# Kernel tuning notes

Hardware: AMD Instinct MI355X
Metric: run time of the kernel (lower is better)

The kernel has to match this reference:

```python
import jax, jax.numpy as jnp
import numpy as np

NUM_NODES = 100000
NUM_EDGES = 1600000
IN_DIM = 128
HID = 128
OUT_DIM = 5


def setup_inputs() -> dict:
    key = jax.random.key(0)
    ks = jax.random.split(key, 8)
    x = jax.random.normal(ks[0], (NUM_NODES, IN_DIM), dtype=jnp.float32)
    edges = jax.random.randint(ks[1], (2, NUM_EDGES), 0, NUM_NODES, dtype=jnp.int32)
    s = 1.0 / np.sqrt(IN_DIM)
    W1 = jax.random.uniform(ks[2], (IN_DIM, HID), jnp.float32, -s, s)
    b1 = jax.random.uniform(ks[3], (HID,), jnp.float32, -s, s)
    sh = 1.0 / np.sqrt(HID)
    W2 = jax.random.uniform(ks[4], (HID, HID), jnp.float32, -sh, sh)
    b2 = jax.random.uniform(ks[5], (HID,), jnp.float32, -sh, sh)
    Wp = jax.random.uniform(ks[6], (HID, OUT_DIM), jnp.float32, -sh, sh)
    bp = jax.random.uniform(ks[7], (OUT_DIM,), jnp.float32, -sh, sh)
    return {"x": x, "edges": edges, "W1": W1, "b1": b1, "W2": W2, "b2": b2, "Wp": Wp, "bp": bp}


def _gnn_layer(x, src, tgt, W, b):
    # scatter-add of source features into targets (mean aggregation)
    agg = jax.ops.segment_sum(x[src], tgt, num_segments=NUM_NODES)  # [N, d]
    cnt = jax.ops.segment_sum(jnp.ones_like(tgt, dtype=x.dtype), tgt, num_segments=NUM_NODES)
    cnt = jnp.maximum(cnt, 1.0)  # clamp(min=1)
    agg = agg / cnt[:, None]
    combined = x + agg  # residual
    return jax.nn.relu(combined @ W + b)


def reference(x, edges, W1, b1, W2, b2, Wp, bp):
    src, tgt = edges[0], edges[1]
    h = _gnn_layer(x, src, tgt, W1, b1)
    h = _gnn_layer(h, src, tgt, W2, b2)
    return h @ Wp + bp  # [N, OUT_DIM]
```

## Files before the change

### kernel.cpp

```cpp
#include <hip/hip_runtime.h>

typedef unsigned int uint32;
typedef unsigned short ushort16;

typedef __attribute__((ext_vector_type(8))) short short8;
typedef __attribute__((ext_vector_type(4))) float f32x4;

#define BMAX 512


__device__ __forceinline__ ushort16 f2bf(float f) {
    uint32 u = __float_as_uint(f);
    u += 0x7fffu + ((u >> 16) & 1u);
    return (ushort16)(u >> 16);
}
__device__ __forceinline__ float bfhi(uint32 u) { return __uint_as_float(u & 0xffff0000u); }
__device__ __forceinline__ float bflo(uint32 u) { return __uint_as_float(u << 16); }
__device__ __forceinline__ uint32 pack2(float a, float b) {
    return (uint32)f2bf(a) | ((uint32)f2bf(b) << 16);
}

union U16 { uint4 u; short8 s; };
__device__ __forceinline__ short8 ld_frag(const ushort16* p) {
    U16 x; x.u = *(const uint4*)p; return x.s;
}

__global__ void prep_wt_kernel(const float* __restrict__ W1, const float* __restrict__ W2,
                               ushort16* __restrict__ Wt1, ushort16* __restrict__ Wt2) {
    const float* W = blockIdx.x ? W2 : W1;
    ushort16* Wt = blockIdx.x ? Wt2 : Wt1;
    for (int i = threadIdx.x; i < 16384; i += 256) {
        int k = i >> 7, c = i & 127;
        Wt[c * 128 + k] = f2bf(W[i]);
    }
}

__global__ __launch_bounds__(256)
void hist_cvt_kernel(const int* __restrict__ tgt, int* __restrict__ hist,
                     const float* __restrict__ x, uint4* __restrict__ xb,
                     int E, int C, int B, int G1, int n64) {
    __shared__ int lh[BMAX];
    int tid = threadIdx.x, blk = blockIdx.x;
    for (int b = tid; b < B; b += 256) lh[b] = 0;
    __syncthreads();
    int e0 = blk * C, e1 = min(e0 + C, E);
    for (int e = e0 + tid; e < e1; e += 256)
        atomicAdd(&lh[tgt[e] >> 8], 1);
    for (int i = blk * 256 + tid; i < n64; i += G1 * 256) {
        const float4* p = (const float4*)x + (size_t)i * 16;
        uint4* q = xb + (size_t)i * 8;
#pragma unroll
        for (int j = 0; j < 8; ++j) {
            float4 a = p[2 * j], bb = p[2 * j + 1];
            uint4 o;
            o.x = pack2(a.x, a.y); o.y = pack2(a.z, a.w);
            o.z = pack2(bb.x, bb.y); o.w = pack2(bb.z, bb.w);
            q[j] = o;
        }
    }
    __syncthreads();
    for (int b = tid; b < B; b += 256) hist[blk * B + b] = lh[b];
}

__global__ __launch_bounds__(256)
void colscan_kernel(int* __restrict__ hist, int* __restrict__ total, int G1, int B) {
    __shared__ int sd[256];
    __shared__ int carrySh;
    int b = blockIdx.x, tid = threadIdx.x;
    if (tid == 0) carrySh = 0;
    __syncthreads();
    for (int g0 = 0; g0 < G1; g0 += 256) {
        int g = g0 + tid;
        int v = (g < G1) ? hist[g * B + b] : 0;
        int c0 = carrySh;
        sd[tid] = v;
        __syncthreads();
        for (int o = 1; o < 256; o <<= 1) {
            int t = (tid >= o) ? sd[tid - o] : 0;
            __syncthreads();
            sd[tid] += t;
            __syncthreads();
        }
        if (g < G1) hist[g * B + b] = sd[tid] - v + c0;
        int tot = sd[255];
        __syncthreads();
        if (tid == 0) carrySh = c0 + tot;
        __syncthreads();
    }
    if (tid == 0) total[b] = carrySh;
}

__global__ __launch_bounds__(512)
void bucketstart_kernel(const int* __restrict__ total, int* __restrict__ bucketStart, int B) {
    __shared__ int sd[512];
    int tid = threadIdx.x;
    int v = (tid < B) ? total[tid] : 0;
    sd[tid] = v;
    __syncthreads();
    for (int o = 1; o < 512; o <<= 1) {
        int t = (tid >= o) ? sd[tid - o] : 0;
        __syncthreads();
        sd[tid] += t;
        __syncthreads();
    }
    if (tid < B) bucketStart[tid] = sd[tid] - v;
    if (tid == 511) bucketStart[B] = sd[511];
}

__global__ __launch_bounds__(256)
void partition_kernel(const int* __restrict__ src, const int* __restrict__ tgt,
                      const int* __restrict__ hist, const int* __restrict__ bucketStart,
                      int2* __restrict__ ebuf, int E, int C, int B) {
    __shared__ int cur[BMAX];
    int tid = threadIdx.x, blk = blockIdx.x;
    for (int b = tid; b < B; b += 256) cur[b] = hist[blk * B + b] + bucketStart[b];
    __syncthreads();
    int e0 = blk * C, e1 = min(e0 + C, E);
    for (int e = e0 + tid; e < e1; e += 256) {
        int t = tgt[e], s = src[e];
        int slot = atomicAdd(&cur[t >> 8], 1);
        int2 p; p.x = t; p.y = s;
        ebuf[slot] = p;
    }
}

__global__ __launch_bounds__(256)
void csr_kernel(const int2* __restrict__ ebuf, const int* __restrict__ bucketStart,
                int* __restrict__ offsets, int* __restrict__ csr, int N, int B, int E) {
    __shared__ int cnt[256];
    __shared__ int sd[256];
    int b = blockIdx.x, tid = threadIdx.x;
    int s = bucketStart[b], e1 = bucketStart[b + 1];
    int n = e1 - s, t0 = b << 8;
    cnt[tid] = 0;
    __syncthreads();
    for (int i = tid; i < n; i += 256) atomicAdd(&cnt[ebuf[s + i].x - t0], 1);
    __syncthreads();
    int v = cnt[tid];
    sd[tid] = v;
    __syncthreads();
    for (int o = 1; o < 256; o <<= 1) {
        int t = (tid >= o) ? sd[tid - o] : 0;
        __syncthreads();
        sd[tid] += t;
        __syncthreads();
    }
    int excl = sd[tid] - v;
    int t = t0 + tid;
    if (t < N) offsets[t] = s + excl;
    if (b == B - 1 && tid == 255) offsets[N] = E;
    __syncthreads();
    cnt[tid] = s + excl;
    __syncthreads();
    for (int i = tid; i < n; i += 256) {
        int2 e = ebuf[s + i];
        int slot = atomicAdd(&cnt[e.x - t0], 1);
        csr[slot] = e.y;
    }
}

__global__ __launch_bounds__(256, 4)
void agg_combine_bf16_kernel(const ushort16* __restrict__ hb,
                             const int* __restrict__ offsets, const int* __restrict__ csr,
                             uint32* __restrict__ outb, int N) {
    int wid = (blockIdx.x * 256 + threadIdx.x) >> 6;
    int lane = threadIdx.x & 63;
    if (wid >= N) return;
    int g = lane >> 4, sl = lane & 15;
    int s0 = offsets[wid];
    int deg = offsets[wid + 1] - s0;
    int fi = sl * 4 + g;
    uint32 su = ((const uint32*)hb)[(size_t)wid * 64 + fi];

    float acc[8];
#pragma unroll
    for (int j = 0; j < 8; ++j) acc[j] = 0.f;

    int base = 0;
    for (; base + 8 <= deg; base += 8) {
        int i0 = csr[s0 + base + g];
        int i1 = csr[s0 + base + 4 + g];
        uint4 v0 = *(const uint4*)(hb + (size_t)i0 * 128 + sl * 8);
        uint4 v1 = *(const uint4*)(hb + (size_t)i1 * 128 + sl * 8);
        acc[0] += bflo(v0.x); acc[1] += bfhi(v0.x);
        acc[2] += bflo(v0.y); acc[3] += bfhi(v0.y);
        acc[4] += bflo(v0.z); acc[5] += bfhi(v0.z);
        acc[6] += bflo(v0.w); acc[7] += bfhi(v0.w);
        acc[0] += bflo(v1.x); acc[1] += bfhi(v1.x);
        acc[2] += bflo(v1.y); acc[3] += bfhi(v1.y);
        acc[4] += bflo(v1.z); acc[5] += bfhi(v1.z);
        acc[6] += bflo(v1.w); acc[7] += bfhi(v1.w);
    }
    for (; base < deg; base += 4) {
        int e = base + g;
        if (e < deg) {
            int s = csr[s0 + e];
            uint4 v = *(const uint4*)(hb + (size_t)s * 128 + sl * 8);
            acc[0] += bflo(v.x); acc[1] += bfhi(v.x);
            acc[2] += bflo(v.y); acc[3] += bfhi(v.y);
            acc[4] += bflo(v.z); acc[5] += bfhi(v.z);
            acc[6] += bflo(v.w); acc[7] += bfhi(v.w);
        }
    }
#pragma unroll
    for (int j = 0; j < 8; ++j) {
        acc[j] += __shfl_xor(acc[j], 16, 64);
        acc[j] += __shfl_xor(acc[j], 32, 64);
    }
    float inv = 1.f / fmaxf((float)deg, 1.f);
    float ax = (g == 0) ? acc[0] : (g == 1) ? acc[2] : (g == 2) ? acc[4] : acc[6];
    float ay = (g == 0) ? acc[1] : (g == 1) ? acc[3] : (g == 2) ? acc[5] : acc[7];
    outb[(size_t)wid * 64 + fi] = pack2(bflo(su) + ax * inv, bfhi(su) + ay * inv);
}

__global__ __launch_bounds__(256)
void gemm_mfma_kernel(const ushort16* __restrict__ A, const ushort16* __restrict__ Wt,
                      const float* __restrict__ bias, int M,
                      ushort16* __restrict__ outB,
                      const float* __restrict__ Wp, const float* __restrict__ bp,
                      float* __restrict__ outP) {
    const int tid = threadIdx.x;
    const int lane = tid & 63;
    const int wave = tid >> 6;
    const int l15 = lane & 15;
    const int quad = lane >> 4;
    const int r0 = blockIdx.x * 64 + wave * 16;

    int arow = r0 + l15;
    if (arow >= M) arow = M - 1;
    const ushort16* aptr = A + (size_t)arow * 128 + quad * 8;
    short8 afr[4];
#pragma unroll
    for (int kt = 0; kt < 4; ++kt) afr[kt] = ld_frag(aptr + kt * 32);

    f32x4 acc[8];
#pragma unroll
    for (int t = 0; t < 8; ++t) acc[t] = (f32x4){0.f, 0.f, 0.f, 0.f};

#pragma unroll
    for (int t = 0; t < 8; ++t) {
        const ushort16* bptr = Wt + (size_t)(16 * t + l15) * 128 + quad * 8;
        short8 b0 = ld_frag(bptr);
        short8 b1 = ld_frag(bptr + 32);
        short8 b2 = ld_frag(bptr + 64);
        short8 b3 = ld_frag(bptr + 96);
        acc[t] = __builtin_amdgcn_mfma_f32_16x16x32_bf16(afr[0], b0, acc[t], 0, 0, 0);
        acc[t] = __builtin_amdgcn_mfma_f32_16x16x32_bf16(afr[1], b1, acc[t], 0, 0, 0);
        acc[t] = __builtin_amdgcn_mfma_f32_16x16x32_bf16(afr[2], b2, acc[t], 0, 0, 0);
        acc[t] = __builtin_amdgcn_mfma_f32_16x16x32_bf16(afr[3], b3, acc[t], 0, 0, 0);
    }

    if (outP) {
        float wpl[8][5];
#pragma unroll
        for (int t = 0; t < 8; ++t)
#pragma unroll
            for (int j = 0; j < 5; ++j) wpl[t][j] = Wp[(16 * t + l15) * 5 + j];
        float p[4][5];
#pragma unroll
        for (int r = 0; r < 4; ++r)
#pragma unroll
            for (int j = 0; j < 5; ++j) p[r][j] = 0.f;
#pragma unroll
        for (int t = 0; t < 8; ++t) {
            float bt = bias[16 * t + l15];
            float ov[4];
            ov[0] = fmaxf(acc[t].x + bt, 0.f);
            ov[1] = fmaxf(acc[t].y + bt, 0.f);
            ov[2] = fmaxf(acc[t].z + bt, 0.f);
            ov[3] = fmaxf(acc[t].w + bt, 0.f);
#pragma unroll
            for (int r = 0; r < 4; ++r)
#pragma unroll
                for (int j = 0; j < 5; ++j) p[r][j] += ov[r] * wpl[t][j];
        }
#pragma unroll
        for (int m = 1; m <= 8; m <<= 1)
#pragma unroll
            for (int r = 0; r < 4; ++r)
#pragma unroll
                for (int j = 0; j < 5; ++j) p[r][j] += __shfl_xor(p[r][j], m, 64);
        if (l15 == 0) {
#pragma unroll
            for (int r = 0; r < 4; ++r) {
                int row = r0 + quad * 4 + r;
                if (row < M) {
#pragma unroll
                    for (int j = 0; j < 5; ++j) outP[(size_t)row * 5 + j] = p[r][j] + bp[j];
                }
            }
        }
    } else {
#pragma unroll
        for (int t = 0; t < 8; ++t) {
            float bt = bias[16 * t + l15];
            float ov[4];
            ov[0] = fmaxf(acc[t].x + bt, 0.f);
            ov[1] = fmaxf(acc[t].y + bt, 0.f);
            ov[2] = fmaxf(acc[t].z + bt, 0.f);
            ov[3] = fmaxf(acc[t].w + bt, 0.f);
#pragma unroll
            for (int r = 0; r < 4; ++r) {
                float nb = __shfl_xor(ov[r], 1, 64);
                int row = r0 + quad * 4 + r;
                if (((l15 & 1) == 0) && row < M) {
                    *(uint32*)(outB + (size_t)row * 128 + 16 * t + l15) = pack2(ov[r], nb);
                }
            }
        }
    }
}

extern "C" void kernel_launch(void* const* d_in, const int* in_sizes, int n_in,
                              void* d_out, int out_size, void* d_ws, size_t ws_size,
                              hipStream_t stream) {
    const float* x     = (const float*)d_in[0];
    const int*   edges = (const int*)d_in[1];
    const float* W1    = (const float*)d_in[2];
    const float* b1    = (const float*)d_in[3];
    const float* W2    = (const float*)d_in[4];
    const float* b2    = (const float*)d_in[5];
    const float* Wp    = (const float*)d_in[6];
    const float* bp    = (const float*)d_in[7];
    float* out = (float*)d_out;

    const int N = in_sizes[0] / 128;
    const int E = in_sizes[1] / 2;
    const int* src = edges;
    const int* tgt = edges + E;

    const int B  = (N + 255) >> 8;
    const int C  = 2048;
    const int G1 = (E + C - 1) / C;
    const int n64 = N * 2;

    char* ws = (char*)d_ws;
    size_t off = 0;
    auto alloc = [&](size_t bytes) {
        char* p = ws + off;
        off = (off + bytes + 255) & ~(size_t)255;
        return p;
    };
    int*      offsets     = (int*)alloc((size_t)(N + 1) * 4);
    int*      csr         = (int*)alloc((size_t)E * 4);
    ushort16* xb          = (ushort16*)alloc((size_t)N * 128 * 2);
    ushort16* hb1         = (ushort16*)alloc((size_t)N * 128 * 2);
    ushort16* bufAb       = (ushort16*)alloc((size_t)N * 128 * 2);
    ushort16* Wt1         = (ushort16*)alloc(128 * 128 * 2);
    ushort16* Wt2         = (ushort16*)alloc(128 * 128 * 2);
    int*      hist        = (int*)alloc((size_t)G1 * B * 4);
    int*      total       = (int*)alloc((size_t)B * 4);
    int*      bucketStart = (int*)alloc((size_t)(B + 1) * 4);
    int2*     ebuf        = (int2*)bufAb;
    (void)ws_size;

    prep_wt_kernel<<<2, 256, 0, stream>>>(W1, W2, Wt1, Wt2);
    hist_cvt_kernel<<<G1, 256, 0, stream>>>(tgt, hist, x, (uint4*)xb, E, C, B, G1, n64);
    colscan_kernel<<<B, 256, 0, stream>>>(hist, total, G1, B);
    bucketstart_kernel<<<1, 512, 0, stream>>>(total, bucketStart, B);
    partition_kernel<<<G1, 256, 0, stream>>>(src, tgt, hist, bucketStart, ebuf, E, C, B);
    csr_kernel<<<B, 256, 0, stream>>>(ebuf, bucketStart, offsets, csr, N, B, E);

    const int aggBlocks  = (N + 3) / 4;
    const int gemmBlocks = (N + 63) / 64;

    agg_combine_bf16_kernel<<<aggBlocks, 256, 0, stream>>>(xb, offsets, csr, (uint32*)bufAb, N);
    gemm_mfma_kernel<<<gemmBlocks, 256, 0, stream>>>(bufAb, Wt1, b1, N, hb1,
                                                     nullptr, nullptr, nullptr);
    agg_combine_bf16_kernel<<<aggBlocks, 256, 0, stream>>>(hb1, offsets, csr, (uint32*)bufAb, N);
    gemm_mfma_kernel<<<gemmBlocks, 256, 0, stream>>>(bufAb, Wt2, b2, N, nullptr,
                                                     Wp, bp, out);
}
```

Measured before the change: 394.2 us.

## Fuse neighbor aggregation into MFMA GEMM via swizzled LDS tile; pack edge buffer

Merges the mean-aggregation kernel and the GEMM kernel into one per-layer kernel. Each block aggregates 64 nodes into an XOR-swizzled shared-memory tile and feeds that tile straight to the MFMA fragments, which removes the round trip of the combined activations through global memory and two launches. The edge partition buffer is packed into 32 bits (local target in the top byte, source in the low 24 bits), halving partition and CSR traffic, and the gather loop is unrolled to 16 edges. In exchange, each wave processes 16 nodes serially, so there are fewer waves in flight to hide gather latency. The 24-bit source packing assumes fewer than 16M nodes.

```diff
diff --git a/kernel.cpp b/kernel.cpp
--- a/kernel.cpp
+++ b/kernel.cpp
@@ -24,6 +24,12 @@
 __device__ __forceinline__ short8 ld_frag(const ushort16* p) {
     U16 x; x.u = *(const uint4*)p; return x.s;
 }
+
+#define ACC8(v) \
+    acc[0] += bflo(v.x); acc[1] += bfhi(v.x); \
+    acc[2] += bflo(v.y); acc[3] += bfhi(v.y); \
+    acc[4] += bflo(v.z); acc[5] += bfhi(v.z); \
+    acc[6] += bflo(v.w); acc[7] += bfhi(v.w);
 
 __global__ void prep_wt_kernel(const float* __restrict__ W1, const float* __restrict__ W2,
                                ushort16* __restrict__ Wt1, ushort16* __restrict__ Wt2) {
@@ -110,7 +116,7 @@
 __global__ __launch_bounds__(256)
 void partition_kernel(const int* __restrict__ src, const int* __restrict__ tgt,
                       const int* __restrict__ hist, const int* __restrict__ bucketStart,
-                      int2* __restrict__ ebuf, int E, int C, int B) {
+                      uint32* __restrict__ ebuf, int E, int C, int B) {
     __shared__ int cur[BMAX];
     int tid = threadIdx.x, blk = blockIdx.x;
     for (int b = tid; b < B; b += 256) cur[b] = hist[blk * B + b] + bucketStart[b];
@@ -119,13 +125,12 @@
     for (int e = e0 + tid; e < e1; e += 256) {
         int t = tgt[e], s = src[e];
         int slot = atomicAdd(&cur[t >> 8], 1);
-        int2 p; p.x = t; p.y = s;
-        ebuf[slot] = p;
+        ebuf[slot] = ((uint32)(t & 255) << 24) | (uint32)s;
     }
 }
 
 __global__ __launch_bounds__(256)
-void csr_kernel(const int2* __restrict__ ebuf, const int* __restrict__ bucketStart,
+void csr_kernel(const uint32* __restrict__ ebuf, const int* __restrict__ bucketStart,
                 int* __restrict__ offsets, int* __restrict__ csr, int N, int B, int E) {
     __shared__ int cnt[256];
     __shared__ int sd[256];
@@ -134,7 +139,7 @@
     int n = e1 - s, t0 = b << 8;
     cnt[tid] = 0;
     __syncthreads();
-    for (int i = tid; i < n; i += 256) atomicAdd(&cnt[ebuf[s + i].x - t0], 1);
+    for (int i = tid; i < n; i += 256) atomicAdd(&cnt[ebuf[s + i] >> 24], 1);
     __syncthreads();
     int v = cnt[tid];
     sd[tid] = v;
@@ -153,85 +158,87 @@
     cnt[tid] = s + excl;
     __syncthreads();
     for (int i = tid; i < n; i += 256) {
-        int2 e = ebuf[s + i];
-        int slot = atomicAdd(&cnt[e.x - t0], 1);
-        csr[slot] = e.y;
+        uint32 e = ebuf[s + i];
+        int slot = atomicAdd(&cnt[e >> 24], 1);
+        csr[slot] = (int)(e & 0x00FFFFFFu);
     }
 }
 
 __global__ __launch_bounds__(256, 4)
-void agg_combine_bf16_kernel(const ushort16* __restrict__ hb,
-                             const int* __restrict__ offsets, const int* __restrict__ csr,
-                             uint32* __restrict__ outb, int N) {
-    int wid = (blockIdx.x * 256 + threadIdx.x) >> 6;
-    int lane = threadIdx.x & 63;
-    if (wid >= N) return;
-    int g = lane >> 4, sl = lane & 15;
-    int s0 = offsets[wid];
-    int deg = offsets[wid + 1] - s0;
-    int fi = sl * 4 + g;
-    uint32 su = ((const uint32*)hb)[(size_t)wid * 64 + fi];
-
-    float acc[8];
-#pragma unroll
-    for (int j = 0; j < 8; ++j) acc[j] = 0.f;
-
-    int base = 0;
-    for (; base + 8 <= deg; base += 8) {
-        int i0 = csr[s0 + base + g];
-        int i1 = csr[s0 + base + 4 + g];
-        uint4 v0 = *(const uint4*)(hb + (size_t)i0 * 128 + sl * 8);
-        uint4 v1 = *(const uint4*)(hb + (size_t)i1 * 128 + sl * 8);
-        acc[0] += bflo(v0.x); acc[1] += bfhi(v0.x);
-        acc[2] += bflo(v0.y); acc[3] += bfhi(v0.y);
-        acc[4] += bflo(v0.z); acc[5] += bfhi(v0.z);
-        acc[6] += bflo(v0.w); acc[7] += bfhi(v0.w);
-        acc[0] += bflo(v1.x); acc[1] += bfhi(v1.x);
-        acc[2] += bflo(v1.y); acc[3] += bfhi(v1.y);
-        acc[4] += bflo(v1.z); acc[5] += bfhi(v1.z);
-        acc[6] += bflo(v1.w); acc[7] += bfhi(v1.w);
-    }
-    for (; base < deg; base += 4) {
-        int e = base + g;
-        if (e < deg) {
-            int s = csr[s0 + e];
-            uint4 v = *(const uint4*)(hb + (size_t)s * 128 + sl * 8);
-            acc[0] += bflo(v.x); acc[1] += bfhi(v.x);
-            acc[2] += bflo(v.y); acc[3] += bfhi(v.y);
-            acc[4] += bflo(v.z); acc[5] += bfhi(v.z);
-            acc[6] += bflo(v.w); acc[7] += bfhi(v.w);
-        }
-    }
-#pragma unroll
-    for (int j = 0; j < 8; ++j) {
-        acc[j] += __shfl_xor(acc[j], 16, 64);
-        acc[j] += __shfl_xor(acc[j], 32, 64);
-    }
-    float inv = 1.f / fmaxf((float)deg, 1.f);
-    float ax = (g == 0) ? acc[0] : (g == 1) ? acc[2] : (g == 2) ? acc[4] : acc[6];
-    float ay = (g == 0) ? acc[1] : (g == 1) ? acc[3] : (g == 2) ? acc[5] : acc[7];
-    outb[(size_t)wid * 64 + fi] = pack2(bflo(su) + ax * inv, bfhi(su) + ay * inv);
-}
-
-__global__ __launch_bounds__(256)
-void gemm_mfma_kernel(const ushort16* __restrict__ A, const ushort16* __restrict__ Wt,
-                      const float* __restrict__ bias, int M,
-                      ushort16* __restrict__ outB,
-                      const float* __restrict__ Wp, const float* __restrict__ bp,
-                      float* __restrict__ outP) {
+void fused_layer_kernel(const ushort16* __restrict__ hb,
+                        const int* __restrict__ offsets, const int* __restrict__ csr,
+                        const ushort16* __restrict__ Wt, const float* __restrict__ bias,
+                        int N,
+                        ushort16* __restrict__ outB,
+                        const float* __restrict__ Wp, const float* __restrict__ bp,
+                        float* __restrict__ outP) {
+    __shared__ uint32 comb[64 * 64];
     const int tid = threadIdx.x;
     const int lane = tid & 63;
     const int wave = tid >> 6;
-    const int l15 = lane & 15;
-    const int quad = lane >> 4;
-    const int r0 = blockIdx.x * 64 + wave * 16;
-
-    int arow = r0 + l15;
-    if (arow >= M) arow = M - 1;
-    const ushort16* aptr = A + (size_t)arow * 128 + quad * 8;
+    const int g = lane >> 4, sl = lane & 15;
+    const int n0 = blockIdx.x * 64;
+
+    for (int i = 0; i < 16; ++i) {
+        int lr = wave * 16 + i;
+        int node = n0 + lr;
+        int chunk = sl ^ (lr & 7);
+        uint32* dst = &comb[lr * 64 + chunk * 4 + g];
+        if (node < N) {
+            int s0 = offsets[node];
+            int deg = offsets[node + 1] - s0;
+            uint32 su = ((const uint32*)hb)[(size_t)node * 64 + sl * 4 + g];
+            float acc[8];
+#pragma unroll
+            for (int j = 0; j < 8; ++j) acc[j] = 0.f;
+            int base = 0;
+            for (; base + 16 <= deg; base += 16) {
+                int i0 = csr[s0 + base + g];
+                int i1 = csr[s0 + base + 4 + g];
+                int i2 = csr[s0 + base + 8 + g];
+                int i3 = csr[s0 + base + 12 + g];
+                uint4 v0 = *(const uint4*)(hb + (size_t)i0 * 128 + sl * 8);
+                uint4 v1 = *(const uint4*)(hb + (size_t)i1 * 128 + sl * 8);
+                uint4 v2 = *(const uint4*)(hb + (size_t)i2 * 128 + sl * 8);
+                uint4 v3 = *(const uint4*)(hb + (size_t)i3 * 128 + sl * 8);
+                ACC8(v0); ACC8(v1); ACC8(v2); ACC8(v3);
+            }
+            for (; base < deg; base += 4) {
+                int e = base + g;
+                if (e < deg) {
+                    int s = csr[s0 + e];
+                    uint4 v = *(const uint4*)(hb + (size_t)s * 128 + sl * 8);
+                    ACC8(v);
+                }
+            }
+#pragma unroll
+            for (int j = 0; j < 8; ++j) {
+                acc[j] += __shfl_xor(acc[j], 16, 64);
+                acc[j] += __shfl_xor(acc[j], 32, 64);
+            }
+            float inv = 1.f / fmaxf((float)deg, 1.f);
+            float ax = (g == 0) ? acc[0] : (g == 1) ? acc[2] : (g == 2) ? acc[4] : acc[6];
+            float ay = (g == 0) ? acc[1] : (g == 1) ? acc[3] : (g == 2) ? acc[5] : acc[7];
+            *dst = pack2(bflo(su) + ax * inv, bfhi(su) + ay * inv);
+        } else {
+            *dst = 0;
+        }
+    }
+    __syncthreads();
+
+    const int l15 = sl;
+    const int quad = g;
+    const int lr0 = wave * 16;
+    const int myrow = lr0 + l15;
+
     short8 afr[4];
 #pragma unroll
-    for (int kt = 0; kt < 4; ++kt) afr[kt] = ld_frag(aptr + kt * 32);
+    for (int kt = 0; kt < 4; ++kt) {
+        int chunk = (quad + kt * 4) ^ (myrow & 7);
+        U16 x;
+        x.u = *(const uint4*)&comb[myrow * 64 + chunk * 4];
+        afr[kt] = x.s;
+    }
 
     f32x4 acc[8];
 #pragma unroll
@@ -251,16 +258,44 @@
     }
 
     if (outP) {
-        float wpl[8][5];
-#pragma unroll
-        for (int t = 0; t < 8; ++t)
-#pragma unroll
-            for (int j = 0; j < 5; ++j) wpl[t][j] = Wp[(16 * t + l15) * 5 + j];
         float p[4][5];
 #pragma unroll
         for (int r = 0; r < 4; ++r)
 #pragma unroll
             for (int j = 0; j < 5; ++j) p[r][j] = 0.f;
+#pragma unroll
+        for (int t = 0; t < 8; ++t) {
+            float wpl[5];
+#pragma unroll
+            for (int j = 0; j < 5; ++j) wpl[j] = Wp[(16 * t + l15) * 5 + j];
+            float bt = bias[16 * t + l15];
+            float ov[4];
+            ov[0] = fmaxf(acc[t].x + bt, 0.f);
+            ov[1] = fmaxf(acc[t].y + bt, 0.f);
+            ov[2] = fmaxf(acc[t].z + bt, 0.f);
+            ov[3] = fmaxf(acc[t].w + bt, 0.f);
+#pragma unroll
+            for (int r = 0; r < 4; ++r)
+#pragma unroll
+                for (int j = 0; j < 5; ++j) p[r][j] += ov[r] * wpl[j];
+        }
+#pragma unroll
+        for (int m = 1; m <= 8; m <<= 1)
+#pragma unroll
+            for (int r = 0; r < 4; ++r)
+#pragma unroll
+                for (int j = 0; j < 5; ++j) p[r][j] += __shfl_xor(p[r][j], m, 64);
+        if (l15 == 0) {
+#pragma unroll
+            for (int r = 0; r < 4; ++r) {
+                int row = n0 + lr0 + quad * 4 + r;
+                if (row < N) {
+#pragma unroll
+                    for (int j = 0; j < 5; ++j) outP[(size_t)row * 5 + j] = p[r][j] + bp[j];
+                }
+            }
+        }
+    } else {
 #pragma unroll
         for (int t = 0; t < 8; ++t) {
             float bt = bias[16 * t + l15];
@@ -270,40 +305,10 @@
             ov[2] = fmaxf(acc[t].z + bt, 0.f);
             ov[3] = fmaxf(acc[t].w + bt, 0.f);
 #pragma unroll
-            for (int r = 0; r < 4; ++r)
-#pragma unroll
-                for (int j = 0; j < 5; ++j) p[r][j] += ov[r] * wpl[t][j];
-        }
-#pragma unroll
-        for (int m = 1; m <= 8; m <<= 1)
-#pragma unroll
-            for (int r = 0; r < 4; ++r)
-#pragma unroll
-                for (int j = 0; j < 5; ++j) p[r][j] += __shfl_xor(p[r][j], m, 64);
-        if (l15 == 0) {
-#pragma unroll
-            for (int r = 0; r < 4; ++r) {
-                int row = r0 + quad * 4 + r;
-                if (row < M) {
-#pragma unroll
-                    for (int j = 0; j < 5; ++j) outP[(size_t)row * 5 + j] = p[r][j] + bp[j];
-                }
-            }
-        }
-    } else {
-#pragma unroll
-        for (int t = 0; t < 8; ++t) {
-            float bt = bias[16 * t + l15];
-            float ov[4];
-            ov[0] = fmaxf(acc[t].x + bt, 0.f);
-            ov[1] = fmaxf(acc[t].y + bt, 0.f);
-            ov[2] = fmaxf(acc[t].z + bt, 0.f);
-            ov[3] = fmaxf(acc[t].w + bt, 0.f);
-#pragma unroll
             for (int r = 0; r < 4; ++r) {
                 float nb = __shfl_xor(ov[r], 1, 64);
-                int row = r0 + quad * 4 + r;
-                if (((l15 & 1) == 0) && row < M) {
+                int row = n0 + lr0 + quad * 4 + r;
+                if (((l15 & 1) == 0) && row < N) {
                     *(uint32*)(outB + (size_t)row * 128 + 16 * t + l15) = pack2(ov[r], nb);
                 }
             }
@@ -345,13 +350,12 @@
     int*      csr         = (int*)alloc((size_t)E * 4);
     ushort16* xb          = (ushort16*)alloc((size_t)N * 128 * 2);
     ushort16* hb1         = (ushort16*)alloc((size_t)N * 128 * 2);
-    ushort16* bufAb       = (ushort16*)alloc((size_t)N * 128 * 2);
     ushort16* Wt1         = (ushort16*)alloc(128 * 128 * 2);
     ushort16* Wt2         = (ushort16*)alloc(128 * 128 * 2);
     int*      hist        = (int*)alloc((size_t)G1 * B * 4);
     int*      total       = (int*)alloc((size_t)B * 4);
     int*      bucketStart = (int*)alloc((size_t)(B + 1) * 4);
-    int2*     ebuf        = (int2*)bufAb;
+    uint32*   ebuf        = (uint32*)alloc((size_t)E * 4);
     (void)ws_size;
 
     prep_wt_kernel<<<2, 256, 0, stream>>>(W1, W2, Wt1, Wt2);
@@ -361,13 +365,10 @@
     partition_kernel<<<G1, 256, 0, stream>>>(src, tgt, hist, bucketStart, ebuf, E, C, B);
     csr_kernel<<<B, 256, 0, stream>>>(ebuf, bucketStart, offsets, csr, N, B, E);
 
-    const int aggBlocks  = (N + 3) / 4;
-    const int gemmBlocks = (N + 63) / 64;
-
-    agg_combine_bf16_kernel<<<aggBlocks, 256, 0, stream>>>(xb, offsets, csr, (uint32*)bufAb, N);
-    gemm_mfma_kernel<<<gemmBlocks, 256, 0, stream>>>(bufAb, Wt1, b1, N, hb1,
-                                                     nullptr, nullptr, nullptr);
-    agg_combine_bf16_kernel<<<aggBlocks, 256, 0, stream>>>(hb1, offsets, csr, (uint32*)bufAb, N);
-    gemm_mfma_kernel<<<gemmBlocks, 256, 0, stream>>>(bufAb, Wt2, b2, N, nullptr,
-                                                     Wp, bp, out);
-}
+    const int fusedBlocks = (N + 63) / 64;
+
+    fused_layer_kernel<<<fusedBlocks, 256, 0, stream>>>(
+        xb, offsets, csr, Wt1, b1, N, hb1, nullptr, nullptr, nullptr);
+    fused_layer_kernel<<<fusedBlocks, 256, 0, stream>>>(
+        hb1, offsets, csr, Wt2, b2, N, nullptr, Wp, bp, out);
+}
```

Measured after the change: 442.6 us. 12.3% more time.

## Fold weight prep and bucket scan into neighbouring kernels; pack edge buffer to 32-bit

Applied to the files above, without the earlier changes.

Merges the weight transpose/convert kernel into the histogram kernel as two extra blocks and removes the separate bucket-start scan kernel. The partition and CSR kernels now each redo the small bucket prefix scan locally. This drops two launches and their serialization gaps. The intermediate edge buffer packs the local target offset (8 bits) with the source index (24 bits) into one uint32, halving its write and read traffic, but this assumes node indices fit in 24 bits. The Wp loads in the GEMM epilogue are also moved inside the loop to cut register pressure.

```diff
diff --git a/kernel.cpp b/kernel.cpp
--- a/kernel.cpp
+++ b/kernel.cpp
@@ -25,22 +25,49 @@
     U16 x; x.u = *(const uint4*)p; return x.s;
 }
 
-__global__ void prep_wt_kernel(const float* __restrict__ W1, const float* __restrict__ W2,
-                               ushort16* __restrict__ Wt1, ushort16* __restrict__ Wt2) {
-    const float* W = blockIdx.x ? W2 : W1;
-    ushort16* Wt = blockIdx.x ? Wt2 : Wt1;
-    for (int i = threadIdx.x; i < 16384; i += 256) {
-        int k = i >> 7, c = i & 127;
-        Wt[c * 128 + k] = f2bf(W[i]);
-    }
-}
-
-__global__ __launch_bounds__(256)
-void hist_cvt_kernel(const int* __restrict__ tgt, int* __restrict__ hist,
-                     const float* __restrict__ x, uint4* __restrict__ xb,
-                     int E, int C, int B, int G1, int n64) {
+#define ACC8(v) \
+    acc[0] += bflo(v.x); acc[1] += bfhi(v.x); \
+    acc[2] += bflo(v.y); acc[3] += bfhi(v.y); \
+    acc[4] += bflo(v.z); acc[5] += bfhi(v.z); \
+    acc[6] += bflo(v.w); acc[7] += bfhi(v.w);
+
+__device__ __forceinline__ void bucket_scan(const int* __restrict__ total, int B,
+                                            int* bs , int* sd ) {
+    int tid = threadIdx.x;
+    int v0 = (2 * tid     < B) ? total[2 * tid]     : 0;
+    int v1 = (2 * tid + 1 < B) ? total[2 * tid + 1] : 0;
+    int s = v0 + v1;
+    sd[tid] = s;
+    __syncthreads();
+    for (int o = 1; o < 256; o <<= 1) {
+        int t = (tid >= o) ? sd[tid - o] : 0;
+        __syncthreads();
+        sd[tid] += t;
+        __syncthreads();
+    }
+    int excl = sd[tid] - s;
+    bs[2 * tid]     = excl;
+    bs[2 * tid + 1] = excl + v0;
+    __syncthreads();
+}
+
+__global__ __launch_bounds__(256)
+void hist_cvt_prep_kernel(const int* __restrict__ tgt, int* __restrict__ hist,
+                          const float* __restrict__ x, uint4* __restrict__ xb,
+                          const float* __restrict__ W1, const float* __restrict__ W2,
+                          ushort16* __restrict__ Wt1, ushort16* __restrict__ Wt2,
+                          int E, int C, int B, int G1, int n64) {
+    int tid = threadIdx.x, blk = blockIdx.x;
+    if (blk >= G1) {
+        const float* W = (blk - G1) ? W2 : W1;
+        ushort16* Wt = (blk - G1) ? Wt2 : Wt1;
+        for (int i = tid; i < 16384; i += 256) {
+            int k = i >> 7, c = i & 127;
+            Wt[c * 128 + k] = f2bf(W[i]);
+        }
+        return;
+    }
     __shared__ int lh[BMAX];
-    int tid = threadIdx.x, blk = blockIdx.x;
     for (int b = tid; b < B; b += 256) lh[b] = 0;
     __syncthreads();
     int e0 = blk * C, e1 = min(e0 + C, E);
@@ -90,51 +117,39 @@
     if (tid == 0) total[b] = carrySh;
 }
 
-__global__ __launch_bounds__(512)
-void bucketstart_kernel(const int* __restrict__ total, int* __restrict__ bucketStart, int B) {
-    __shared__ int sd[512];
-    int tid = threadIdx.x;
-    int v = (tid < B) ? total[tid] : 0;
-    sd[tid] = v;
-    __syncthreads();
-    for (int o = 1; o < 512; o <<= 1) {
-        int t = (tid >= o) ? sd[tid - o] : 0;
-        __syncthreads();
-        sd[tid] += t;
-        __syncthreads();
-    }
-    if (tid < B) bucketStart[tid] = sd[tid] - v;
-    if (tid == 511) bucketStart[B] = sd[511];
-}
-
 __global__ __launch_bounds__(256)
 void partition_kernel(const int* __restrict__ src, const int* __restrict__ tgt,
-                      const int* __restrict__ hist, const int* __restrict__ bucketStart,
-                      int2* __restrict__ ebuf, int E, int C, int B) {
+                      const int* __restrict__ hist, const int* __restrict__ total,
+                      uint32* __restrict__ ebuf, int E, int C, int B) {
+    __shared__ int bs[512];
+    __shared__ int sd[256];
     __shared__ int cur[BMAX];
     int tid = threadIdx.x, blk = blockIdx.x;
-    for (int b = tid; b < B; b += 256) cur[b] = hist[blk * B + b] + bucketStart[b];
+    bucket_scan(total, B, bs, sd);
+    for (int b = tid; b < B; b += 256) cur[b] = hist[blk * B + b] + bs[b];
     __syncthreads();
     int e0 = blk * C, e1 = min(e0 + C, E);
     for (int e = e0 + tid; e < e1; e += 256) {
         int t = tgt[e], s = src[e];
         int slot = atomicAdd(&cur[t >> 8], 1);
-        int2 p; p.x = t; p.y = s;
-        ebuf[slot] = p;
-    }
-}
-
-__global__ __launch_bounds__(256)
-void csr_kernel(const int2* __restrict__ ebuf, const int* __restrict__ bucketStart,
+        ebuf[slot] = ((uint32)(t & 255) << 24) | (uint32)s;
+    }
+}
+
+__global__ __launch_bounds__(256)
+void csr_kernel(const uint32* __restrict__ ebuf, const int* __restrict__ total,
                 int* __restrict__ offsets, int* __restrict__ csr, int N, int B, int E) {
+    __shared__ int bs[512];
+    __shared__ int sd[256];
     __shared__ int cnt[256];
-    __shared__ int sd[256];
     int b = blockIdx.x, tid = threadIdx.x;
-    int s = bucketStart[b], e1 = bucketStart[b + 1];
-    int n = e1 - s, t0 = b << 8;
+    bucket_scan(total, B, bs, sd);
+    int s = bs[b];
+    int n = bs[b + 1] - s;
+    int t0 = b << 8;
     cnt[tid] = 0;
     __syncthreads();
-    for (int i = tid; i < n; i += 256) atomicAdd(&cnt[ebuf[s + i].x - t0], 1);
+    for (int i = tid; i < n; i += 256) atomicAdd(&cnt[ebuf[s + i] >> 24], 1);
     __syncthreads();
     int v = cnt[tid];
     sd[tid] = v;
@@ -153,9 +168,9 @@
     cnt[tid] = s + excl;
     __syncthreads();
     for (int i = tid; i < n; i += 256) {
-        int2 e = ebuf[s + i];
-        int slot = atomicAdd(&cnt[e.x - t0], 1);
-        csr[slot] = e.y;
+        uint32 e = ebuf[s + i];
+        int slot = atomicAdd(&cnt[e >> 24], 1);
+        csr[slot] = (int)(e & 0x00FFFFFFu);
     }
 }
 
@@ -182,24 +197,14 @@
         int i1 = csr[s0 + base + 4 + g];
         uint4 v0 = *(const uint4*)(hb + (size_t)i0 * 128 + sl * 8);
         uint4 v1 = *(const uint4*)(hb + (size_t)i1 * 128 + sl * 8);
-        acc[0] += bflo(v0.x); acc[1] += bfhi(v0.x);
-        acc[2] += bflo(v0.y); acc[3] += bfhi(v0.y);
-        acc[4] += bflo(v0.z); acc[5] += bfhi(v0.z);
-        acc[6] += bflo(v0.w); acc[7] += bfhi(v0.w);
-        acc[0] += bflo(v1.x); acc[1] += bfhi(v1.x);
-        acc[2] += bflo(v1.y); acc[3] += bfhi(v1.y);
-        acc[4] += bflo(v1.z); acc[5] += bfhi(v1.z);
-        acc[6] += bflo(v1.w); acc[7] += bfhi(v1.w);
+        ACC8(v0); ACC8(v1);
     }
     for (; base < deg; base += 4) {
         int e = base + g;
         if (e < deg) {
             int s = csr[s0 + e];
             uint4 v = *(const uint4*)(hb + (size_t)s * 128 + sl * 8);
-            acc[0] += bflo(v.x); acc[1] += bfhi(v.x);
-            acc[2] += bflo(v.y); acc[3] += bfhi(v.y);
-            acc[4] += bflo(v.z); acc[5] += bfhi(v.z);
-            acc[6] += bflo(v.w); acc[7] += bfhi(v.w);
+            ACC8(v);
         }
     }
 #pragma unroll
@@ -251,11 +256,6 @@
     }
 
     if (outP) {
-        float wpl[8][5];
-#pragma unroll
-        for (int t = 0; t < 8; ++t)
-#pragma unroll
-            for (int j = 0; j < 5; ++j) wpl[t][j] = Wp[(16 * t + l15) * 5 + j];
         float p[4][5];
 #pragma unroll
         for (int r = 0; r < 4; ++r)
@@ -263,6 +263,9 @@
             for (int j = 0; j < 5; ++j) p[r][j] = 0.f;
 #pragma unroll
         for (int t = 0; t < 8; ++t) {
+            float wpl[5];
+#pragma unroll
+            for (int j = 0; j < 5; ++j) wpl[j] = Wp[(16 * t + l15) * 5 + j];
             float bt = bias[16 * t + l15];
             float ov[4];
             ov[0] = fmaxf(acc[t].x + bt, 0.f);
@@ -272,7 +275,7 @@
 #pragma unroll
             for (int r = 0; r < 4; ++r)
 #pragma unroll
-                for (int j = 0; j < 5; ++j) p[r][j] += ov[r] * wpl[t][j];
+                for (int j = 0; j < 5; ++j) p[r][j] += ov[r] * wpl[j];
         }
 #pragma unroll
         for (int m = 1; m <= 8; m <<= 1)
@@ -341,25 +344,23 @@
         off = (off + bytes + 255) & ~(size_t)255;
         return p;
     };
-    int*      offsets     = (int*)alloc((size_t)(N + 1) * 4);
-    int*      csr         = (int*)alloc((size_t)E * 4);
-    ushort16* xb          = (ushort16*)alloc((size_t)N * 128 * 2);
-    ushort16* hb1         = (ushort16*)alloc((size_t)N * 128 * 2);
-    ushort16* bufAb       = (ushort16*)alloc((size_t)N * 128 * 2);
-    ushort16* Wt1         = (ushort16*)alloc(128 * 128 * 2);
-    ushort16* Wt2         = (ushort16*)alloc(128 * 128 * 2);
-    int*      hist        = (int*)alloc((size_t)G1 * B * 4);
-    int*      total       = (int*)alloc((size_t)B * 4);
-    int*      bucketStart = (int*)alloc((size_t)(B + 1) * 4);
-    int2*     ebuf        = (int2*)bufAb;
+    int*      offsets = (int*)alloc((size_t)(N + 1) * 4);
+    int*      csr     = (int*)alloc((size_t)E * 4);
+    ushort16* xb      = (ushort16*)alloc((size_t)N * 128 * 2);
+    ushort16* hb1     = (ushort16*)alloc((size_t)N * 128 * 2);
+    ushort16* bufAb   = (ushort16*)alloc((size_t)N * 128 * 2);
+    ushort16* Wt1     = (ushort16*)alloc(128 * 128 * 2);
+    ushort16* Wt2     = (ushort16*)alloc(128 * 128 * 2);
+    int*      hist    = (int*)alloc((size_t)G1 * B * 4);
+    int*      total   = (int*)alloc((size_t)B * 4);
+    uint32*   ebuf    = (uint32*)bufAb;
     (void)ws_size;
 
-    prep_wt_kernel<<<2, 256, 0, stream>>>(W1, W2, Wt1, Wt2);
-    hist_cvt_kernel<<<G1, 256, 0, stream>>>(tgt, hist, x, (uint4*)xb, E, C, B, G1, n64);
+    hist_cvt_prep_kernel<<<G1 + 2, 256, 0, stream>>>(tgt, hist, x, (uint4*)xb,
+                                                     W1, W2, Wt1, Wt2, E, C, B, G1, n64);
     colscan_kernel<<<B, 256, 0, stream>>>(hist, total, G1, B);
-    bucketstart_kernel<<<1, 512, 0, stream>>>(total, bucketStart, B);
-    partition_kernel<<<G1, 256, 0, stream>>>(src, tgt, hist, bucketStart, ebuf, E, C, B);
-    csr_kernel<<<B, 256, 0, stream>>>(ebuf, bucketStart, offsets, csr, N, B, E);
+    partition_kernel<<<G1, 256, 0, stream>>>(src, tgt, hist, total, ebuf, E, C, B);
+    csr_kernel<<<B, 256, 0, stream>>>(ebuf, total, offsets, csr, N, B, E);
 
     const int aggBlocks  = (N + 3) / 4;
     const int gemmBlocks = (N + 63) / 64;
```

Result: faster. 380.3 us (-3.5%).
